# Optimization experiments

Hardware: AMD Instinct MI355X
Metric: run time of the kernel (lower is better)

Reference implementation:

```python
import jax, jax.numpy as jnp
import numpy as np

IN_Q = 256   # in_features // 4
OUT_Q = 256  # out_features // 4


def setup_inputs() -> dict:
    key = jax.random.key(0)
    kx, kr, ki, kj, kk = jax.random.split(key, 5)
    stdv = 1.0 / np.sqrt(IN_Q)
    return {
        "x": jax.random.normal(kx, (4, 8192, IN_Q * 4), dtype=jnp.float32),
        "r_weight": jax.random.uniform(kr, (OUT_Q, IN_Q), minval=-stdv, maxval=stdv, dtype=jnp.float32),
        "i_weight": jax.random.uniform(ki, (OUT_Q, IN_Q), minval=-stdv, maxval=stdv, dtype=jnp.float32),
        "j_weight": jax.random.uniform(kj, (OUT_Q, IN_Q), minval=-stdv, maxval=stdv, dtype=jnp.float32),
        "k_weight": jax.random.uniform(kk, (OUT_Q, IN_Q), minval=-stdv, maxval=stdv, dtype=jnp.float32),
        "bias": jnp.zeros((OUT_Q * 4,), dtype=jnp.float32),
    }


def reference(x, r_weight, i_weight, j_weight, k_weight, bias):
    batch_dims = x.shape[:-1]
    xq = x.reshape(*batch_dims, IN_Q, 4)  # [..., in_q, 4]
    r_x, i_x, j_x, k_x = xq[..., 0], xq[..., 1], xq[..., 2], xq[..., 3]

    lin = lambda v, w: jnp.einsum('...i,oi->...o', v, w)  # F.linear, no bias

    out_r = lin(r_x, r_weight) - lin(i_x, i_weight) - lin(j_x, j_weight) - lin(k_x, k_weight)
    out_i = lin(r_x, i_weight) + lin(i_x, r_weight) + lin(j_x, k_weight) - lin(k_x, j_weight)
    out_j = lin(r_x, j_weight) - lin(i_x, k_weight) + lin(j_x, r_weight) + lin(k_x, i_weight)
    out_k = lin(r_x, k_weight) + lin(i_x, j_weight) - lin(j_x, i_weight) + lin(k_x, r_weight)

    out = jnp.stack([out_r, out_i, out_j, out_k], axis=-1)  # [..., out_q, 4]
    out = out.reshape(*batch_dims, OUT_Q * 4)
    return out + bias
```

## Files before the change

### kernel.cpp

```cpp
#include <hip/hip_runtime.h>


typedef __attribute__((ext_vector_type(8))) short bf16x8;
typedef __attribute__((ext_vector_type(4))) float f32x4;

#define M_TOT 32768
#define N_TOT 1024
#define K_TOT 1024
#define BM 256
#define BN 256
#define BK 64
#define NKT (K_TOT / BK)

__device__ __forceinline__ unsigned short f2bf(float f) {
    union { float f; unsigned int u; } v; v.f = f;
    unsigned int u = v.u;
    u += 0x7fffu + ((u >> 16) & 1u);
    return (unsigned short)(u >> 16);
}

__global__ __launch_bounds__(256) void cvt_x(const float4* __restrict__ x,
                                             ushort4* __restrict__ y) {
    int idx = blockIdx.x * 256 + threadIdx.x;
    float4 a = x[idx];
    ushort4 o;
    o.x = f2bf(a.x); o.y = f2bf(a.y); o.z = f2bf(a.z); o.w = f2bf(a.w);
    y[idx] = o;
}

__global__ __launch_bounds__(256) void build_w(const float* __restrict__ R,
                                               const float* __restrict__ I,
                                               const float* __restrict__ J,
                                               const float* __restrict__ Kw,
                                               ushort4* __restrict__ Wb) {
    int n = blockIdx.x;
    int i = threadIdx.x;
    int o = n >> 2, co = n & 3;
    int base = o * 256 + i;
    float r = R[base], ii = I[base], j = J[base], k = Kw[base];
    float v0, v1, v2, v3;
    if (co == 0)      { v0 = r;  v1 = -ii; v2 = -j;  v3 = -k; }
    else if (co == 1) { v0 = ii; v1 = r;   v2 = k;   v3 = -j; }
    else if (co == 2) { v0 = j;  v1 = -k;  v2 = r;   v3 = ii; }
    else              { v0 = k;  v1 = j;   v2 = -ii; v3 = r;  }
    ushort4 w;
    w.x = f2bf(v0); w.y = f2bf(v1); w.z = f2bf(v2); w.w = f2bf(v3);
    Wb[n * 256 + i] = w;
}

__device__ __forceinline__ void async_lds16(const void* g, void* l) {
    __builtin_amdgcn_global_load_lds(
        (const __attribute__((address_space(1))) unsigned int*)g,
        (__attribute__((address_space(3))) unsigned int*)l,
        16, 0, 0);
}

__device__ __forceinline__ void stage_ht(const unsigned short* __restrict__ G,
                                         int row0, int k0,
                                         unsigned short* ht,
                                         int wave, int lane) {
    int sr = lane >> 2;
    int sc = ((lane & 3) * 8) ^ ((lane & 32) ? 16 : 0);
#pragma unroll
    for (int j = 0; j < 2; ++j) {
        int si = j * 8 + wave;
        int rg = si >> 1, cg = si & 1;
        async_lds16(G + (size_t)(row0 + rg * 16 + sr) * K_TOT + k0 + cg * 32 + sc,
                    ht + si * 512);
    }
}

__device__ __forceinline__ bf16x8 frag_ld(const unsigned short* ht,
                                          int row, int kk, int quad) {
    int idx = (((row >> 4) << 1) + (kk >> 5)) * 512 + (row & 15) * 32 + quad * 8;
    idx ^= (row & 8) << 1;
    return *(const bf16x8*)(ht + idx);
}

__global__ __launch_bounds__(512, 2) void gemm_bt(
        const unsigned short* __restrict__ A,
        const unsigned short* __restrict__ B,
        const float* __restrict__ bias,
        float* __restrict__ C) {
    __shared__ unsigned short smem[2][2][2][8192];

    const int tid  = threadIdx.x;
    const int wave = tid >> 6;
    const int lane = tid & 63;
    const int quad = lane >> 4;
    const int r16  = lane & 15;
    const int wm   = wave & 1;
    const int wn   = wave >> 1;

    int bid = blockIdx.x;
    int wg  = (bid & 7) * 64 + (bid >> 3);
    const int m0 = (wg >> 2) * BM;
    const int n0 = (wg & 3) * BN;

    f32x4 acc[8][4];
#pragma unroll
    for (int i = 0; i < 8; ++i)
#pragma unroll
        for (int j = 0; j < 4; ++j)
            acc[i][j] = (f32x4){0.f, 0.f, 0.f, 0.f};

    const int brow0 = (wn & 1) * 64;

    stage_ht(A, m0,        0, &smem[0][0][0][0], wave, lane);
    stage_ht(A, m0 + 128,  0, &smem[0][0][1][0], wave, lane);
    stage_ht(B, n0,        0, &smem[0][1][0][0], wave, lane);
    stage_ht(B, n0 + 128,  0, &smem[0][1][1][0], wave, lane);
    stage_ht(A, m0,       BK, &smem[1][0][0][0], wave, lane);
    stage_ht(A, m0 + 128, BK, &smem[1][0][1][0], wave, lane);
    asm volatile("s_waitcnt vmcnt(4)" ::: "memory");
    __builtin_amdgcn_s_barrier();

    bf16x8 af[4][2], bl[2][2], bh[2][2];

#pragma unroll 2
    for (int t = 0; t < NKT; ++t) {
        const int c = t & 1;
        const unsigned short* Ah = &smem[c][0][wm][0];
        const unsigned short* Bh = &smem[c][1][wn >> 1][0];

#pragma unroll
        for (int mb = 0; mb < 4; ++mb) {
            af[mb][0] = frag_ld(Ah, mb * 16 + r16, 0, quad);
            af[mb][1] = frag_ld(Ah, mb * 16 + r16, 32, quad);
        }
#pragma unroll
        for (int nb = 0; nb < 2; ++nb) {
            bl[nb][0] = frag_ld(Bh, brow0 + nb * 16 + r16, 0, quad);
            bl[nb][1] = frag_ld(Bh, brow0 + nb * 16 + r16, 32, quad);
        }
        if (t + 1 < NKT) {
            stage_ht(B, n0,       (t + 1) * BK, &smem[c ^ 1][1][0][0], wave, lane);
            stage_ht(B, n0 + 128, (t + 1) * BK, &smem[c ^ 1][1][1][0], wave, lane);
        }
        __builtin_amdgcn_s_barrier();
        asm volatile("s_waitcnt lgkmcnt(0)" ::: "memory");
        __builtin_amdgcn_s_setprio(1);
#pragma unroll
        for (int mb = 0; mb < 4; ++mb)
#pragma unroll
            for (int nb = 0; nb < 2; ++nb) {
                acc[mb][nb] = __builtin_amdgcn_mfma_f32_16x16x32_bf16(
                    af[mb][0], bl[nb][0], acc[mb][nb], 0, 0, 0);
                acc[mb][nb] = __builtin_amdgcn_mfma_f32_16x16x32_bf16(
                    af[mb][1], bl[nb][1], acc[mb][nb], 0, 0, 0);
            }
        __builtin_amdgcn_s_setprio(0);
        __builtin_amdgcn_s_barrier();

#pragma unroll
        for (int nb = 0; nb < 2; ++nb) {
            bh[nb][0] = frag_ld(Bh, brow0 + (nb + 2) * 16 + r16, 0, quad);
            bh[nb][1] = frag_ld(Bh, brow0 + (nb + 2) * 16 + r16, 32, quad);
        }
        __builtin_amdgcn_s_barrier();
        asm volatile("s_waitcnt lgkmcnt(0)" ::: "memory");
        __builtin_amdgcn_s_setprio(1);
#pragma unroll
        for (int mb = 0; mb < 4; ++mb)
#pragma unroll
            for (int nb = 0; nb < 2; ++nb) {
                acc[mb][nb + 2] = __builtin_amdgcn_mfma_f32_16x16x32_bf16(
                    af[mb][0], bh[nb][0], acc[mb][nb + 2], 0, 0, 0);
                acc[mb][nb + 2] = __builtin_amdgcn_mfma_f32_16x16x32_bf16(
                    af[mb][1], bh[nb][1], acc[mb][nb + 2], 0, 0, 0);
            }
        __builtin_amdgcn_s_setprio(0);
        __builtin_amdgcn_s_barrier();

#pragma unroll
        for (int mb = 0; mb < 4; ++mb) {
            af[mb][0] = frag_ld(Ah, 64 + mb * 16 + r16, 0, quad);
            af[mb][1] = frag_ld(Ah, 64 + mb * 16 + r16, 32, quad);
        }
        __builtin_amdgcn_s_barrier();
        asm volatile("s_waitcnt lgkmcnt(0)" ::: "memory");
        __builtin_amdgcn_s_setprio(1);
#pragma unroll
        for (int mb = 0; mb < 4; ++mb)
#pragma unroll
            for (int nb = 0; nb < 2; ++nb) {
                acc[mb + 4][nb + 2] = __builtin_amdgcn_mfma_f32_16x16x32_bf16(
                    af[mb][0], bh[nb][0], acc[mb + 4][nb + 2], 0, 0, 0);
                acc[mb + 4][nb + 2] = __builtin_amdgcn_mfma_f32_16x16x32_bf16(
                    af[mb][1], bh[nb][1], acc[mb + 4][nb + 2], 0, 0, 0);
            }
        __builtin_amdgcn_s_setprio(0);
        __builtin_amdgcn_s_barrier();

        if (t + 2 < NKT) {
            stage_ht(A, m0,       (t + 2) * BK, &smem[c][0][0][0], wave, lane);
            stage_ht(A, m0 + 128, (t + 2) * BK, &smem[c][0][1][0], wave, lane);
        }
        __builtin_amdgcn_s_barrier();
        __builtin_amdgcn_s_setprio(1);
#pragma unroll
        for (int mb = 0; mb < 4; ++mb)
#pragma unroll
            for (int nb = 0; nb < 2; ++nb) {
                acc[mb + 4][nb] = __builtin_amdgcn_mfma_f32_16x16x32_bf16(
                    af[mb][0], bl[nb][0], acc[mb + 4][nb], 0, 0, 0);
                acc[mb + 4][nb] = __builtin_amdgcn_mfma_f32_16x16x32_bf16(
                    af[mb][1], bl[nb][1], acc[mb + 4][nb], 0, 0, 0);
            }
        __builtin_amdgcn_s_setprio(0);
        if (t + 2 < NKT) {
            asm volatile("s_waitcnt vmcnt(4)" ::: "memory");
        } else if (t + 1 < NKT) {
            asm volatile("s_waitcnt vmcnt(0)" ::: "memory");
        }
        __builtin_amdgcn_s_barrier();
    }

    const int mbase = m0 + wm * 128 + quad * 4;
    const int nbase = n0 + wn * 64 + r16;
#pragma unroll
    for (int nb = 0; nb < 4; ++nb) {
        int col  = nbase + nb * 16;
        float bv = bias[col];
#pragma unroll
        for (int mb = 0; mb < 8; ++mb) {
            int rowb = mbase + mb * 16;
            f32x4 v  = acc[mb][nb];
#pragma unroll
            for (int r = 0; r < 4; ++r)
                C[(size_t)(rowb + r) * N_TOT + col] = v[r] + bv;
        }
    }
}

extern "C" void kernel_launch(void* const* d_in, const int* in_sizes, int n_in,
                              void* d_out, int out_size, void* d_ws, size_t ws_size,
                              hipStream_t stream) {
    const float* x    = (const float*)d_in[0];
    const float* rw   = (const float*)d_in[1];
    const float* iw   = (const float*)d_in[2];
    const float* jw   = (const float*)d_in[3];
    const float* kw   = (const float*)d_in[4];
    const float* bias = (const float*)d_in[5];
    float* out = (float*)d_out;

    unsigned short* xb = (unsigned short*)d_ws;
    unsigned short* Wb = (unsigned short*)((char*)d_ws + (size_t)M_TOT * K_TOT * 2);

    cvt_x<<<(M_TOT * (size_t)K_TOT) / 4 / 256, 256, 0, stream>>>(
        (const float4*)x, (ushort4*)xb);

    build_w<<<N_TOT, 256, 0, stream>>>(rw, iw, jw, kw, (ushort4*)Wb);

    gemm_bt<<<dim3((M_TOT / BM) * (N_TOT / BN)), 512, 0, stream>>>(
        xb, Wb, bias, out);
}
```

Baseline: 324.9 us.

## Fuse fp32-to-bf16 conversion of x into GEMM A-tile staging

Removes the separate cvt_x kernel and its bf16 round-trip through global memory. The GEMM now loads fp32 x directly into registers, converts it to bf16 and writes it swizzled into LDS, with a register prefetch pipeline spread across the k-loop phases. Fragment address computation is also hoisted into precomputed per-lane base pointers. In exchange it adds register pressure and extra VMEM traffic inside the GEMM. Each x tile is also reconverted by the four blocks that share it across N.

```diff
diff --git a/kernel.cpp b/kernel.cpp
--- a/kernel.cpp
+++ b/kernel.cpp
@@ -19,13 +19,13 @@
     return (unsigned short)(u >> 16);
 }
 
-__global__ __launch_bounds__(256) void cvt_x(const float4* __restrict__ x,
-                                             ushort4* __restrict__ y) {
-    int idx = blockIdx.x * 256 + threadIdx.x;
-    float4 a = x[idx];
-    ushort4 o;
-    o.x = f2bf(a.x); o.y = f2bf(a.y); o.z = f2bf(a.z); o.w = f2bf(a.w);
-    y[idx] = o;
+__device__ __forceinline__ bf16x8 cvt8(float4 a, float4 b) {
+    bf16x8 r;
+    r[0] = (short)f2bf(a.x); r[1] = (short)f2bf(a.y);
+    r[2] = (short)f2bf(a.z); r[3] = (short)f2bf(a.w);
+    r[4] = (short)f2bf(b.x); r[5] = (short)f2bf(b.y);
+    r[6] = (short)f2bf(b.z); r[7] = (short)f2bf(b.w);
+    return r;
 }
 
 __global__ __launch_bounds__(256) void build_w(const float* __restrict__ R,
@@ -70,19 +70,13 @@
     }
 }
 
-__device__ __forceinline__ bf16x8 frag_ld(const unsigned short* ht,
-                                          int row, int kk, int quad) {
-    int idx = (((row >> 4) << 1) + (kk >> 5)) * 512 + (row & 15) * 32 + quad * 8;
-    idx ^= (row & 8) << 1;
-    return *(const bf16x8*)(ht + idx);
-}
-
-__global__ __launch_bounds__(512, 2) void gemm_bt(
-        const unsigned short* __restrict__ A,
+__global__ __launch_bounds__(512, 2) void gemm_fused(
+        const float* __restrict__ X,
         const unsigned short* __restrict__ B,
         const float* __restrict__ bias,
         float* __restrict__ C) {
-    __shared__ unsigned short smem[2][2][2][8192];
+    __shared__ unsigned short smemA[2][2][8192];
+    __shared__ unsigned short smemB[2][2][8192];
 
     const int tid  = threadIdx.x;
     const int wave = tid >> 6;
@@ -97,6 +91,20 @@
     const int m0 = (wg >> 2) * BM;
     const int n0 = (wg & 3) * BN;
 
+    const int laneRd = (r16 * 32 + quad * 8) ^ ((r16 & 8) << 1);
+    const unsigned short* baseA = &smemA[0][wm][0] + laneRd;
+    const unsigned short* baseB = &smemB[0][wn >> 1][0] + (wn & 1) * 4096 + laneRd;
+
+    const int qrow = tid >> 2;
+    const int ah   = qrow >> 6;
+    const int r64  = qrow & 63;
+    const int kb   = (tid & 3) * 16;
+    const int wTerm = ah * 8192 +
+        (((r64 >> 4) * 2 + (kb >> 5)) * 512 +
+         ((((r64 & 15) * 32) + (kb & 31)) ^ ((r64 & 8) << 1)));
+    unsigned short* baseW = &smemA[0][0][0] + wTerm;
+    const float* gA = X + (size_t)(m0 + ah * 128 + r64) * K_TOT + kb;
+
     f32x4 acc[8][4];
 #pragma unroll
     for (int i = 0; i < 8; ++i)
@@ -104,38 +112,65 @@
         for (int j = 0; j < 4; ++j)
             acc[i][j] = (f32x4){0.f, 0.f, 0.f, 0.f};
 
-    const int brow0 = (wn & 1) * 64;
-
-    stage_ht(A, m0,        0, &smem[0][0][0][0], wave, lane);
-    stage_ht(A, m0 + 128,  0, &smem[0][0][1][0], wave, lane);
-    stage_ht(B, n0,        0, &smem[0][1][0][0], wave, lane);
-    stage_ht(B, n0 + 128,  0, &smem[0][1][1][0], wave, lane);
-    stage_ht(A, m0,       BK, &smem[1][0][0][0], wave, lane);
-    stage_ht(A, m0 + 128, BK, &smem[1][0][1][0], wave, lane);
-    asm volatile("s_waitcnt vmcnt(4)" ::: "memory");
-    __builtin_amdgcn_s_barrier();
+    float4 aq0, aq1, aq2, aq3;
+    float4 bq0, bq1, bq2, bq3;
+
+    {
+        float4 p0 = *(const float4*)(gA + 0);
+        float4 p1 = *(const float4*)(gA + 4);
+        float4 p2 = *(const float4*)(gA + 8);
+        float4 p3 = *(const float4*)(gA + 12);
+        float4 q0 = *(const float4*)(gA + 65536 + 0);
+        float4 q1 = *(const float4*)(gA + 65536 + 4);
+        float4 q2 = *(const float4*)(gA + 65536 + 8);
+        float4 q3 = *(const float4*)(gA + 65536 + 12);
+        stage_ht(B, n0,       0, &smemB[0][0][0], wave, lane);
+        stage_ht(B, n0 + 128, 0, &smemB[0][1][0], wave, lane);
+        *(bf16x8*)(baseW + 0)        = cvt8(p0, p1);
+        *(bf16x8*)(baseW + 8)        = cvt8(p2, p3);
+        *(bf16x8*)(baseW + 4096)     = cvt8(q0, q1);
+        *(bf16x8*)(baseW + 4096 + 8) = cvt8(q2, q3);
+        p0 = *(const float4*)(gA + BK + 0);
+        p1 = *(const float4*)(gA + BK + 4);
+        p2 = *(const float4*)(gA + BK + 8);
+        p3 = *(const float4*)(gA + BK + 12);
+        q0 = *(const float4*)(gA + 65536 + BK + 0);
+        q1 = *(const float4*)(gA + 65536 + BK + 4);
+        q2 = *(const float4*)(gA + 65536 + BK + 8);
+        q3 = *(const float4*)(gA + 65536 + BK + 12);
+        *(bf16x8*)(baseW + 16384)        = cvt8(p0, p1);
+        *(bf16x8*)(baseW + 16384 + 8)    = cvt8(p2, p3);
+        *(bf16x8*)(baseW + 20480)        = cvt8(q0, q1);
+        *(bf16x8*)(baseW + 20480 + 8)    = cvt8(q2, q3);
+        aq0 = *(const float4*)(gA + 2 * BK + 0);
+        aq1 = *(const float4*)(gA + 2 * BK + 4);
+        aq2 = *(const float4*)(gA + 2 * BK + 8);
+        aq3 = *(const float4*)(gA + 2 * BK + 12);
+        asm volatile("s_waitcnt vmcnt(4)" ::: "memory");
+        asm volatile("s_waitcnt lgkmcnt(0)" ::: "memory");
+        __builtin_amdgcn_s_barrier();
+    }
 
     bf16x8 af[4][2], bl[2][2], bh[2][2];
 
 #pragma unroll 2
     for (int t = 0; t < NKT; ++t) {
-        const int c = t & 1;
-        const unsigned short* Ah = &smem[c][0][wm][0];
-        const unsigned short* Bh = &smem[c][1][wn >> 1][0];
+        const int c  = t & 1;
+        const int cA = c * 16384;
 
 #pragma unroll
         for (int mb = 0; mb < 4; ++mb) {
-            af[mb][0] = frag_ld(Ah, mb * 16 + r16, 0, quad);
-            af[mb][1] = frag_ld(Ah, mb * 16 + r16, 32, quad);
+            af[mb][0] = *(const bf16x8*)(baseA + cA + (mb * 2 + 0) * 512);
+            af[mb][1] = *(const bf16x8*)(baseA + cA + (mb * 2 + 1) * 512);
         }
 #pragma unroll
         for (int nb = 0; nb < 2; ++nb) {
-            bl[nb][0] = frag_ld(Bh, brow0 + nb * 16 + r16, 0, quad);
-            bl[nb][1] = frag_ld(Bh, brow0 + nb * 16 + r16, 32, quad);
+            bl[nb][0] = *(const bf16x8*)(baseB + cA + (nb * 2 + 0) * 512);
+            bl[nb][1] = *(const bf16x8*)(baseB + cA + (nb * 2 + 1) * 512);
         }
         if (t + 1 < NKT) {
-            stage_ht(B, n0,       (t + 1) * BK, &smem[c ^ 1][1][0][0], wave, lane);
-            stage_ht(B, n0 + 128, (t + 1) * BK, &smem[c ^ 1][1][1][0], wave, lane);
+            stage_ht(B, n0,       (t + 1) * BK, &smemB[c ^ 1][0][0], wave, lane);
+            stage_ht(B, n0 + 128, (t + 1) * BK, &smemB[c ^ 1][1][0], wave, lane);
         }
         __builtin_amdgcn_s_barrier();
         asm volatile("s_waitcnt lgkmcnt(0)" ::: "memory");
@@ -154,8 +189,17 @@
 
 #pragma unroll
         for (int nb = 0; nb < 2; ++nb) {
-            bh[nb][0] = frag_ld(Bh, brow0 + (nb + 2) * 16 + r16, 0, quad);
-            bh[nb][1] = frag_ld(Bh, brow0 + (nb + 2) * 16 + r16, 32, quad);
+            bh[nb][0] = *(const bf16x8*)(baseB + cA + ((nb + 2) * 2 + 0) * 512);
+            bh[nb][1] = *(const bf16x8*)(baseB + cA + ((nb + 2) * 2 + 1) * 512);
+        }
+        if (t + 2 < NKT) {
+            const int k2 = (t + 2) * BK;
+            *(bf16x8*)(baseW + cA + 0) = cvt8(aq0, aq1);
+            *(bf16x8*)(baseW + cA + 8) = cvt8(aq2, aq3);
+            bq0 = *(const float4*)(gA + 65536 + k2 + 0);
+            bq1 = *(const float4*)(gA + 65536 + k2 + 4);
+            bq2 = *(const float4*)(gA + 65536 + k2 + 8);
+            bq3 = *(const float4*)(gA + 65536 + k2 + 12);
         }
         __builtin_amdgcn_s_barrier();
         asm volatile("s_waitcnt lgkmcnt(0)" ::: "memory");
@@ -174,8 +218,15 @@
 
 #pragma unroll
         for (int mb = 0; mb < 4; ++mb) {
-            af[mb][0] = frag_ld(Ah, 64 + mb * 16 + r16, 0, quad);
-            af[mb][1] = frag_ld(Ah, 64 + mb * 16 + r16, 32, quad);
+            af[mb][0] = *(const bf16x8*)(baseA + cA + ((mb + 4) * 2 + 0) * 512);
+            af[mb][1] = *(const bf16x8*)(baseA + cA + ((mb + 4) * 2 + 1) * 512);
+        }
+        if (t + 3 < NKT) {
+            const int k3 = (t + 3) * BK;
+            aq0 = *(const float4*)(gA + k3 + 0);
+            aq1 = *(const float4*)(gA + k3 + 4);
+            aq2 = *(const float4*)(gA + k3 + 8);
+            aq3 = *(const float4*)(gA + k3 + 12);
         }
         __builtin_amdgcn_s_barrier();
         asm volatile("s_waitcnt lgkmcnt(0)" ::: "memory");
@@ -192,11 +243,6 @@
         __builtin_amdgcn_s_setprio(0);
         __builtin_amdgcn_s_barrier();
 
-        if (t + 2 < NKT) {
-            stage_ht(A, m0,       (t + 2) * BK, &smem[c][0][0][0], wave, lane);
-            stage_ht(A, m0 + 128, (t + 2) * BK, &smem[c][0][1][0], wave, lane);
-        }
-        __builtin_amdgcn_s_barrier();
         __builtin_amdgcn_s_setprio(1);
 #pragma unroll
         for (int mb = 0; mb < 4; ++mb)
@@ -209,10 +255,13 @@
             }
         __builtin_amdgcn_s_setprio(0);
         if (t + 2 < NKT) {
+            *(bf16x8*)(baseW + cA + 4096)     = cvt8(bq0, bq1);
+            *(bf16x8*)(baseW + cA + 4096 + 8) = cvt8(bq2, bq3);
             asm volatile("s_waitcnt vmcnt(4)" ::: "memory");
         } else if (t + 1 < NKT) {
             asm volatile("s_waitcnt vmcnt(0)" ::: "memory");
         }
+        asm volatile("s_waitcnt lgkmcnt(0)" ::: "memory");
         __builtin_amdgcn_s_barrier();
     }
 
@@ -244,14 +293,10 @@
     const float* bias = (const float*)d_in[5];
     float* out = (float*)d_out;
 
-    unsigned short* xb = (unsigned short*)d_ws;
-    unsigned short* Wb = (unsigned short*)((char*)d_ws + (size_t)M_TOT * K_TOT * 2);
-
-    cvt_x<<<(M_TOT * (size_t)K_TOT) / 4 / 256, 256, 0, stream>>>(
-        (const float4*)x, (ushort4*)xb);
+    unsigned short* Wb = (unsigned short*)d_ws;
 
     build_w<<<N_TOT, 256, 0, stream>>>(rw, iw, jw, kw, (ushort4*)Wb);
 
-    gemm_bt<<<dim3((M_TOT / BM) * (N_TOT / BN)), 512, 0, stream>>>(
-        xb, Wb, bias, out);
-}
+    gemm_fused<<<dim3((M_TOT / BM) * (N_TOT / BN)), 512, 0, stream>>>(
+        x, Wb, bias, out);
+}
```

Measured after the change: 315.3 us. -3.0%, faster.
